# Kernel tuning notes

Hardware: AMD Instinct MI355X
Metric: run time of the kernel (lower is better)

## Reference

```python
import jax, jax.numpy as jnp
import numpy as np

DIM = 256
NUM_HEADS = 8
HEAD_DIM = DIM // NUM_HEADS
SCALE = 1.0 / DIM ** 0.5  # NOTE: source scales by 1/sqrt(dim), not 1/sqrt(head_dim)


def setup_inputs() -> dict:
    key = jax.random.key(0)
    k_x, k_wqkv, k_wout = jax.random.split(key, 3)
    x = jax.random.normal(k_x, (4, 2048, DIM), dtype=jnp.float32)
    # xavier_uniform for Linear(dim, 3*dim): limit = sqrt(6/(fan_in+fan_out))
    lim_qkv = float(np.sqrt(6.0 / (DIM + 3 * DIM)))
    w_qkv = jax.random.uniform(k_wqkv, (3 * DIM, DIM), minval=-lim_qkv, maxval=lim_qkv, dtype=jnp.float32)
    b_qkv = jnp.zeros((3 * DIM,), dtype=jnp.float32)
    lim_out = float(np.sqrt(6.0 / (DIM + DIM)))
    w_out = jax.random.uniform(k_wout, (DIM, DIM), minval=-lim_out, maxval=lim_out, dtype=jnp.float32)
    b_out = jnp.zeros((DIM,), dtype=jnp.float32)
    return {"x": x, "w_qkv": w_qkv, "b_qkv": b_qkv, "w_out": w_out, "b_out": b_out}


def reference(x, w_qkv, b_qkv, w_out, b_out):
    B, N, C = x.shape
    H, D = NUM_HEADS, C // NUM_HEADS
    qkv = x @ w_qkv.T + b_qkv                       # [B, N, 3C]
    qkv = qkv.reshape(B, N, 3, H, D)
    q = qkv[:, :, 0].transpose(0, 2, 1, 3)          # [B, H, N, D]
    k = qkv[:, :, 1].transpose(0, 2, 1, 3)
    v = qkv[:, :, 2].transpose(0, 2, 1, 3)
    attn = jnp.einsum("bhnd,bhmd->bhnm", q, k) * SCALE  # [B, H, N, N]
    attn = jax.nn.softmax(attn, axis=-1)
    z = jnp.einsum("bhnm,bhmd->bhnd", attn, v)      # [B, H, N, D]
    z = z.transpose(0, 2, 1, 3).reshape(B, N, C)
    return z @ w_out.T + b_out
```

## Files before the change

kernel.cpp:

```cpp
#include <hip/hip_runtime.h>


#define SEQ 2048
#define BATCH 4
#define NHEADS 8
#define HDIM 32
#define DIMC 256
#define SCALE_LOG2E 0.09016844005556021f

typedef __attribute__((ext_vector_type(8))) short short8;
typedef __attribute__((ext_vector_type(4))) float f32x4;

union BF8 { unsigned u[4]; short8 s8; };

__device__ __forceinline__ unsigned pk2bf(float a, float b) {
    union { float f; unsigned u; } ua, ub;
    ua.f = a; ub.f = b;
    return __builtin_amdgcn_perm(ub.u + 0x8000u, ua.u + 0x8000u, 0x07060302u);
}
__device__ __forceinline__ short f2bf(float a) {
    union { float f; unsigned u; } x; x.f = a;
    return (short)((x.u + 0x8000u) >> 16);
}

__global__ __launch_bounds__(256) void qkv_fused(const float* __restrict__ X,
                                                 const float* __restrict__ W,
                                                 const float* __restrict__ bias,
                                                 short* __restrict__ Q,
                                                 short* __restrict__ Kd,
                                                 short* __restrict__ V) {
    __shared__ __align__(16) union SM {
        struct { short A[128][72]; short B[64][72]; } ab;
        short CQ[128][72];
        short CV[64][136];
    } sm;

    const int m0 = blockIdx.y * 128, bx = blockIdx.x;
    const int n0 = bx * 64;
    const int tid = threadIdx.x;
    const int w = tid >> 6, lane = tid & 63;
    const int m = lane & 15, g = lane >> 4;
    const int wr = w >> 1, wc = w & 1;

    const int arow = tid >> 1, acol = (tid & 1) * 32;
    const int brow = tid >> 2, bcol = (tid & 3) * 16;

    f32x4 acc[4][2] = {};

    for (int kt = 0; kt < DIMC; kt += 64) {
        const float* xp = &X[(size_t)(m0 + arow) * DIMC + kt + acol];
        const float* wp = &W[(size_t)(n0 + brow) * DIMC + kt + bcol];
        float4 xv[8], wv[4];
#pragma unroll
        for (int i = 0; i < 8; i++) xv[i] = *(const float4*)(xp + i * 4);
#pragma unroll
        for (int i = 0; i < 4; i++) wv[i] = *(const float4*)(wp + i * 4);
        __syncthreads();
#pragma unroll
        for (int i = 0; i < 4; i++) {
            BF8 c;
            c.u[0] = pk2bf(xv[i * 2].x, xv[i * 2].y);
            c.u[1] = pk2bf(xv[i * 2].z, xv[i * 2].w);
            c.u[2] = pk2bf(xv[i * 2 + 1].x, xv[i * 2 + 1].y);
            c.u[3] = pk2bf(xv[i * 2 + 1].z, xv[i * 2 + 1].w);
            *(short8*)&sm.ab.A[arow][acol + i * 8] = c.s8;
        }
#pragma unroll
        for (int i = 0; i < 2; i++) {
            BF8 c;
            c.u[0] = pk2bf(wv[i * 2].x, wv[i * 2].y);
            c.u[1] = pk2bf(wv[i * 2].z, wv[i * 2].w);
            c.u[2] = pk2bf(wv[i * 2 + 1].x, wv[i * 2 + 1].y);
            c.u[3] = pk2bf(wv[i * 2 + 1].z, wv[i * 2 + 1].w);
            *(short8*)&sm.ab.B[brow][bcol + i * 8] = c.s8;
        }
        __syncthreads();
#pragma unroll
        for (int kk = 0; kk < 2; kk++) {
            short8 af[4], bf[2];
#pragma unroll
            for (int mt = 0; mt < 4; mt++)
                af[mt] = *(const short8*)&sm.ab.A[wr * 64 + mt * 16 + m][kk * 32 + g * 8];
#pragma unroll
            for (int nt = 0; nt < 2; nt++)
                bf[nt] = *(const short8*)&sm.ab.B[wc * 32 + nt * 16 + m][kk * 32 + g * 8];
#pragma unroll
            for (int mt = 0; mt < 4; mt++)
#pragma unroll
                for (int nt = 0; nt < 2; nt++)
                    acc[mt][nt] = __builtin_amdgcn_mfma_f32_16x16x32_bf16(af[mt], bf[nt], acc[mt][nt], 0, 0, 0);
        }
    }

    const int which = bx >> 2;
    const int h0 = (bx & 3) * 2;
    const int bidx = blockIdx.y >> 4;
    const int ntok0 = (blockIdx.y & 15) * 128;
    float bv[2];
#pragma unroll
    for (int nt = 0; nt < 2; nt++) bv[nt] = bias[n0 + wc * 32 + nt * 16 + m];

    __syncthreads();
    if (which != 2) {
        const float qs = (which == 0) ? SCALE_LOG2E : 1.0f;
#pragma unroll
        for (int mt = 0; mt < 4; mt++)
#pragma unroll
            for (int nt = 0; nt < 2; nt++)
#pragma unroll
                for (int r = 0; r < 4; r++)
                    sm.CQ[wr * 64 + mt * 16 + g * 4 + r][wc * 32 + nt * 16 + m] =
                        f2bf((acc[mt][nt][r] + bv[nt]) * qs);
        __syncthreads();
        short* dst = (which == 0) ? Q : Kd;
        const int tok = tid >> 1, d0 = (tid & 1) * 16;
#pragma unroll
        for (int hh = 0; hh < 2; hh++) {
            size_t o = ((size_t)((bidx * NHEADS + h0 + hh) * SEQ) + ntok0 + tok) * HDIM + d0;
            *(short8*)&dst[o] = *(const short8*)&sm.CQ[tok][hh * 32 + d0];
            *(short8*)&dst[o + 8] = *(const short8*)&sm.CQ[tok][hh * 32 + d0 + 8];
        }
    } else {
#pragma unroll
        for (int mt = 0; mt < 4; mt++)
#pragma unroll
            for (int nt = 0; nt < 2; nt++) {
                uint2 p;
                p.x = pk2bf(acc[mt][nt][0] + bv[nt], acc[mt][nt][1] + bv[nt]);
                p.y = pk2bf(acc[mt][nt][2] + bv[nt], acc[mt][nt][3] + bv[nt]);
                *(uint2*)&sm.CV[wc * 32 + nt * 16 + m][wr * 64 + mt * 16 + g * 4] = p;
            }
        __syncthreads();
        const int col = tid >> 2, t0 = (tid & 3) * 32;
        const int hh = col >> 5, d = col & 31;
        size_t o = ((size_t)((bidx * NHEADS + h0 + hh) * HDIM) + d) * SEQ + ntok0 + t0;
#pragma unroll
        for (int c2 = 0; c2 < 4; c2++)
            *(short8*)&V[o + c2 * 8] = *(const short8*)&sm.CV[col][t0 + c2 * 8];
    }
}

__global__ __launch_bounds__(256) void attn_tile(const short* __restrict__ Q,
                                                 const short* __restrict__ K,
                                                 const short* __restrict__ V,
                                                 short* __restrict__ Zb) {
    __shared__ __align__(16) union SM {
        struct { short Ks[2][128][40]; short Vs[2][32][136]; } kv;
        struct { float O[4][64][36]; float L[4][64]; } ep;
    } sm;

    const int bh = blockIdx.y;
    const int b = bh >> 3, h = bh & 7;
    const int q0 = blockIdx.x * 64;
    const short* qb = Q + (size_t)bh * SEQ * HDIM;
    const short* kb = K + (size_t)bh * SEQ * HDIM;
    const short* vb = V + (size_t)bh * HDIM * SEQ;
    const int tid = threadIdx.x;
    const int w = tid >> 6, lane = tid & 63;
    const int m = lane & 15, g = lane >> 4;

    short8 qfr[4];
#pragma unroll
    for (int qt = 0; qt < 4; qt++)
        qfr[qt] = *(const short8*)(qb + (size_t)(q0 + qt * 16 + m) * HDIM + g * 8);

    const int krow = tid >> 1, kcol = (tid & 1) * 16;
    const int rl = krow & 31;
    const int lrow = (krow & ~31) | (((rl >> 2) & 1) << 4) | ((rl >> 3) << 2) | (rl & 3);
    const int vrow = tid >> 3, vcol = (tid & 7) * 16;

    f32x4 o[4][2] = {};
    f32x4 ol[4] = {};
    const short8 ones = {0x3F80, 0x3F80, 0x3F80, 0x3F80, 0x3F80, 0x3F80, 0x3F80, 0x3F80};

    short8 k0a = *(const short8*)(kb + (size_t)krow * HDIM + kcol);
    short8 k0b = *(const short8*)(kb + (size_t)krow * HDIM + kcol + 8);
    short8 v0a = *(const short8*)(vb + (size_t)vrow * SEQ + vcol);
    short8 v0b = *(const short8*)(vb + (size_t)vrow * SEQ + vcol + 8);
    *(short8*)&sm.kv.Ks[0][lrow][kcol] = k0a;
    *(short8*)&sm.kv.Ks[0][lrow][kcol + 8] = k0b;
    *(short8*)&sm.kv.Vs[0][vrow][vcol] = v0a;
    *(short8*)&sm.kv.Vs[0][vrow][vcol + 8] = v0b;
    __syncthreads();

    for (int it = 0; it < SEQ / 128; ++it) {
        const int buf = it & 1;
        if (it < SEQ / 128 - 1) {
            const int kn = (it + 1) * 128;
            k0a = *(const short8*)(kb + (size_t)(kn + krow) * HDIM + kcol);
            k0b = *(const short8*)(kb + (size_t)(kn + krow) * HDIM + kcol + 8);
            v0a = *(const short8*)(vb + (size_t)vrow * SEQ + kn + vcol);
            v0b = *(const short8*)(vb + (size_t)vrow * SEQ + kn + vcol + 8);
        }

        short8 kf0 = *(const short8*)&sm.kv.Ks[buf][w * 32 + m][g * 8];
        short8 kf1 = *(const short8*)&sm.kv.Ks[buf][w * 32 + 16 + m][g * 8];
        short8 vf0 = *(const short8*)&sm.kv.Vs[buf][m][w * 32 + g * 8];
        short8 vf1 = *(const short8*)&sm.kv.Vs[buf][16 + m][w * 32 + g * 8];

#pragma unroll
        for (int qt = 0; qt < 4; qt++) {
            f32x4 z4 = {0.f, 0.f, 0.f, 0.f};
            f32x4 st0 = __builtin_amdgcn_mfma_f32_16x16x32_bf16(kf0, qfr[qt], z4, 0, 0, 0);
            f32x4 st1 = __builtin_amdgcn_mfma_f32_16x16x32_bf16(kf1, qfr[qt], z4, 0, 0, 0);
            BF8 a;
            a.u[0] = pk2bf(__builtin_amdgcn_exp2f(st0[0]), __builtin_amdgcn_exp2f(st0[1]));
            a.u[1] = pk2bf(__builtin_amdgcn_exp2f(st0[2]), __builtin_amdgcn_exp2f(st0[3]));
            a.u[2] = pk2bf(__builtin_amdgcn_exp2f(st1[0]), __builtin_amdgcn_exp2f(st1[1]));
            a.u[3] = pk2bf(__builtin_amdgcn_exp2f(st1[2]), __builtin_amdgcn_exp2f(st1[3]));
            o[qt][0] = __builtin_amdgcn_mfma_f32_16x16x32_bf16(a.s8, vf0, o[qt][0], 0, 0, 0);
            o[qt][1] = __builtin_amdgcn_mfma_f32_16x16x32_bf16(a.s8, vf1, o[qt][1], 0, 0, 0);
            ol[qt] = __builtin_amdgcn_mfma_f32_16x16x32_bf16(a.s8, ones, ol[qt], 0, 0, 0);
        }

        if (it < SEQ / 128 - 1) {
            const int nb = buf ^ 1;
            *(short8*)&sm.kv.Ks[nb][lrow][kcol] = k0a;
            *(short8*)&sm.kv.Ks[nb][lrow][kcol + 8] = k0b;
            *(short8*)&sm.kv.Vs[nb][vrow][vcol] = v0a;
            *(short8*)&sm.kv.Vs[nb][vrow][vcol + 8] = v0b;
        }
        __syncthreads();
    }

#pragma unroll
    for (int qt = 0; qt < 4; qt++) {
#pragma unroll
        for (int dh = 0; dh < 2; dh++)
#pragma unroll
            for (int r = 0; r < 4; r++)
                sm.ep.O[w][qt * 16 + g * 4 + r][dh * 16 + m] = o[qt][dh][r];
        if (m == 0)
#pragma unroll
            for (int r = 0; r < 4; r++)
                sm.ep.L[w][qt * 16 + g * 4 + r] = ol[qt][r];
    }
    __syncthreads();

    const int ql = tid >> 2, d0 = (tid & 3) * 8;
    float lt = sm.ep.L[0][ql] + sm.ep.L[1][ql] + sm.ep.L[2][ql] + sm.ep.L[3][ql];
    float inv = __builtin_amdgcn_rcpf(lt);
    float sv[8];
#pragma unroll
    for (int j = 0; j < 8; j++)
        sv[j] = sm.ep.O[0][ql][d0 + j] + sm.ep.O[1][ql][d0 + j] +
                sm.ep.O[2][ql][d0 + j] + sm.ep.O[3][ql][d0 + j];
    BF8 pz;
#pragma unroll
    for (int j = 0; j < 4; j++)
        pz.u[j] = pk2bf(sv[2 * j] * inv, sv[2 * j + 1] * inv);
    *(short8*)&Zb[(size_t)(b * SEQ + q0 + ql) * DIMC + h * HDIM + d0] = pz.s8;
}

__global__ __launch_bounds__(256) void out_fused(const short* __restrict__ A,
                                                 const float* __restrict__ W,
                                                 const float* __restrict__ bias,
                                                 float* __restrict__ C) {
    __shared__ __align__(16) short As[64][72];
    __shared__ __align__(16) short Bs[64][72];
    const int m0 = blockIdx.y * 64, n0 = blockIdx.x * 64;
    const int tid = threadIdx.x;
    const int w = tid >> 6, lane = tid & 63;
    const int m = lane & 15, g = lane >> 4;
    const int srow = tid >> 2, scol = (tid & 3) * 16;

    f32x4 acc[4] = {};

    for (int kt = 0; kt < DIMC; kt += 64) {
        short8 a0 = *(const short8*)&A[(size_t)(m0 + srow) * DIMC + kt + scol];
        short8 a1 = *(const short8*)&A[(size_t)(m0 + srow) * DIMC + kt + scol + 8];
        const float* wp = &W[(size_t)(n0 + srow) * DIMC + kt + scol];
        float4 wv[4];
#pragma unroll
        for (int i = 0; i < 4; i++) wv[i] = *(const float4*)(wp + i * 4);
        __syncthreads();
        *(short8*)&As[srow][scol] = a0;
        *(short8*)&As[srow][scol + 8] = a1;
#pragma unroll
        for (int i = 0; i < 2; i++) {
            BF8 c;
            c.u[0] = pk2bf(wv[i * 2].x, wv[i * 2].y);
            c.u[1] = pk2bf(wv[i * 2].z, wv[i * 2].w);
            c.u[2] = pk2bf(wv[i * 2 + 1].x, wv[i * 2 + 1].y);
            c.u[3] = pk2bf(wv[i * 2 + 1].z, wv[i * 2 + 1].w);
            *(short8*)&Bs[srow][scol + i * 8] = c.s8;
        }
        __syncthreads();
#pragma unroll
        for (int kk = 0; kk < 2; kk++) {
            short8 af = *(const short8*)&As[w * 16 + m][kk * 32 + g * 8];
#pragma unroll
            for (int nt = 0; nt < 4; nt++) {
                short8 bf = *(const short8*)&Bs[nt * 16 + m][kk * 32 + g * 8];
                acc[nt] = __builtin_amdgcn_mfma_f32_16x16x32_bf16(af, bf, acc[nt], 0, 0, 0);
            }
        }
    }

    float bv[4];
#pragma unroll
    for (int nt = 0; nt < 4; nt++) bv[nt] = bias[n0 + nt * 16 + m];
#pragma unroll
    for (int nt = 0; nt < 4; nt++)
#pragma unroll
        for (int r = 0; r < 4; r++)
            C[(size_t)(m0 + w * 16 + g * 4 + r) * DIMC + n0 + nt * 16 + m] = acc[nt][r] + bv[nt];
}

extern "C" void kernel_launch(void* const* d_in, const int* in_sizes, int n_in,
                              void* d_out, int out_size, void* d_ws, size_t ws_size,
                              hipStream_t stream) {
    const float* x     = (const float*)d_in[0];
    const float* w_qkv = (const float*)d_in[1];
    const float* b_qkv = (const float*)d_in[2];
    const float* w_out = (const float*)d_in[3];
    const float* b_out = (const float*)d_in[4];
    float* out = (float*)d_out;

    const size_t HSZ = (size_t)BATCH * NHEADS * SEQ * HDIM;
    short* qw = (short*)d_ws;
    short* kw = qw + HSZ;
    short* vw = kw + HSZ;
    short* zb = vw + HSZ;

    qkv_fused<<<dim3(12, 64), 256, 0, stream>>>(x, w_qkv, b_qkv, qw, kw, vw);
    attn_tile<<<dim3(32, 32), 256, 0, stream>>>(qw, kw, vw, zb);
    out_fused<<<dim3(4, 128), 256, 0, stream>>>(zb, w_out, b_out, out);
}
```

Baseline: 131.7 us.

## Pre-convert inputs and weights to bf16 and register-prefetch GEMM tiles

Adds a separate kernel that converts x, w_qkv and w_out to bf16 once, so the QKV and output GEMMs load bf16 directly instead of converting fp32 inside every tile. Both GEMMs now prefetch the next K tile into registers while the current tile is computed, overlapping global loads with MFMA work. This costs an extra launch plus an fp32 read and bf16 write of x (about 8 MB of traffic), which could outweigh the per-tile conversion it removes, since x is read by 12 column blocks in the QKV kernel.

Measured after the change: 120.0 us. -8.9%, faster.

```diff
diff --git a/kernel.cpp b/kernel.cpp
--- a/kernel.cpp
+++ b/kernel.cpp
@@ -23,12 +23,36 @@
     return (short)((x.u + 0x8000u) >> 16);
 }
 
-__global__ __launch_bounds__(256) void qkv_fused(const float* __restrict__ X,
-                                                 const float* __restrict__ W,
-                                                 const float* __restrict__ bias,
-                                                 short* __restrict__ Q,
-                                                 short* __restrict__ Kd,
-                                                 short* __restrict__ V) {
+#define NX (BATCH * SEQ * DIMC)
+#define NQW (3 * DIMC * DIMC)
+#define NOW (DIMC * DIMC)
+
+__global__ __launch_bounds__(256) void cvt_bf16(const float* __restrict__ x,
+                                                const float* __restrict__ wq,
+                                                const float* __restrict__ wo,
+                                                short* __restrict__ xb,
+                                                short* __restrict__ wqb,
+                                                short* __restrict__ wob) {
+    int i = (blockIdx.x * 256 + threadIdx.x) * 4;
+    const float* src;
+    short* dst;
+    int off;
+    if (i < NX) { src = x; dst = xb; off = i; }
+    else if (i < NX + NQW) { src = wq; dst = wqb; off = i - NX; }
+    else { src = wo; dst = wob; off = i - NX - NQW; }
+    float4 v = *(const float4*)&src[off];
+    uint2 p;
+    p.x = pk2bf(v.x, v.y);
+    p.y = pk2bf(v.z, v.w);
+    *(uint2*)&dst[off] = p;
+}
+
+__global__ __launch_bounds__(256) void qkv_mfma(const short* __restrict__ Xb,
+                                                const short* __restrict__ Wb,
+                                                const float* __restrict__ bias,
+                                                short* __restrict__ Q,
+                                                short* __restrict__ Kd,
+                                                short* __restrict__ V) {
     __shared__ __align__(16) union SM {
         struct { short A[128][72]; short B[64][72]; } ab;
         short CQ[128][72];
@@ -47,34 +71,28 @@
 
     f32x4 acc[4][2] = {};
 
+    const short* ap = Xb + (size_t)(m0 + arow) * DIMC + acol;
+    const short* bp = Wb + (size_t)(n0 + brow) * DIMC + bcol;
+
+    short8 pa[4], pb[2];
+#pragma unroll
+    for (int i = 0; i < 4; i++) pa[i] = *(const short8*)(ap + i * 8);
+#pragma unroll
+    for (int i = 0; i < 2; i++) pb[i] = *(const short8*)(bp + i * 8);
+
     for (int kt = 0; kt < DIMC; kt += 64) {
-        const float* xp = &X[(size_t)(m0 + arow) * DIMC + kt + acol];
-        const float* wp = &W[(size_t)(n0 + brow) * DIMC + kt + bcol];
-        float4 xv[8], wv[4];
-#pragma unroll
-        for (int i = 0; i < 8; i++) xv[i] = *(const float4*)(xp + i * 4);
-#pragma unroll
-        for (int i = 0; i < 4; i++) wv[i] = *(const float4*)(wp + i * 4);
-        __syncthreads();
-#pragma unroll
-        for (int i = 0; i < 4; i++) {
-            BF8 c;
-            c.u[0] = pk2bf(xv[i * 2].x, xv[i * 2].y);
-            c.u[1] = pk2bf(xv[i * 2].z, xv[i * 2].w);
-            c.u[2] = pk2bf(xv[i * 2 + 1].x, xv[i * 2 + 1].y);
-            c.u[3] = pk2bf(xv[i * 2 + 1].z, xv[i * 2 + 1].w);
-            *(short8*)&sm.ab.A[arow][acol + i * 8] = c.s8;
-        }
-#pragma unroll
-        for (int i = 0; i < 2; i++) {
-            BF8 c;
-            c.u[0] = pk2bf(wv[i * 2].x, wv[i * 2].y);
-            c.u[1] = pk2bf(wv[i * 2].z, wv[i * 2].w);
-            c.u[2] = pk2bf(wv[i * 2 + 1].x, wv[i * 2 + 1].y);
-            c.u[3] = pk2bf(wv[i * 2 + 1].z, wv[i * 2 + 1].w);
-            *(short8*)&sm.ab.B[brow][bcol + i * 8] = c.s8;
-        }
-        __syncthreads();
+        __syncthreads();
+#pragma unroll
+        for (int i = 0; i < 4; i++) *(short8*)&sm.ab.A[arow][acol + i * 8] = pa[i];
+#pragma unroll
+        for (int i = 0; i < 2; i++) *(short8*)&sm.ab.B[brow][bcol + i * 8] = pb[i];
+        __syncthreads();
+        if (kt + 64 < DIMC) {
+#pragma unroll
+            for (int i = 0; i < 4; i++) pa[i] = *(const short8*)(ap + kt + 64 + i * 8);
+#pragma unroll
+            for (int i = 0; i < 2; i++) pb[i] = *(const short8*)(bp + kt + 64 + i * 8);
+        }
 #pragma unroll
         for (int kk = 0; kk < 2; kk++) {
             short8 af[4], bf[2];
@@ -252,10 +270,10 @@
     *(short8*)&Zb[(size_t)(b * SEQ + q0 + ql) * DIMC + h * HDIM + d0] = pz.s8;
 }
 
-__global__ __launch_bounds__(256) void out_fused(const short* __restrict__ A,
-                                                 const float* __restrict__ W,
-                                                 const float* __restrict__ bias,
-                                                 float* __restrict__ C) {
+__global__ __launch_bounds__(256) void out_mfma(const short* __restrict__ A,
+                                                const short* __restrict__ Wb,
+                                                const float* __restrict__ bias,
+                                                float* __restrict__ C) {
     __shared__ __align__(16) short As[64][72];
     __shared__ __align__(16) short Bs[64][72];
     const int m0 = blockIdx.y * 64, n0 = blockIdx.x * 64;
@@ -266,26 +284,31 @@
 
     f32x4 acc[4] = {};
 
+    const short* ap = A + (size_t)(m0 + srow) * DIMC + scol;
+    const short* bp = Wb + (size_t)(n0 + srow) * DIMC + scol;
+
+    short8 pa[2], pb[2];
+#pragma unroll
+    for (int i = 0; i < 2; i++) {
+        pa[i] = *(const short8*)(ap + i * 8);
+        pb[i] = *(const short8*)(bp + i * 8);
+    }
+
     for (int kt = 0; kt < DIMC; kt += 64) {
-        short8 a0 = *(const short8*)&A[(size_t)(m0 + srow) * DIMC + kt + scol];
-        short8 a1 = *(const short8*)&A[(size_t)(m0 + srow) * DIMC + kt + scol + 8];
-        const float* wp = &W[(size_t)(n0 + srow) * DIMC + kt + scol];
-        float4 wv[4];
-#pragma unroll
-        for (int i = 0; i < 4; i++) wv[i] = *(const float4*)(wp + i * 4);
-        __syncthreads();
-        *(short8*)&As[srow][scol] = a0;
-        *(short8*)&As[srow][scol + 8] = a1;
+        __syncthreads();
 #pragma unroll
         for (int i = 0; i < 2; i++) {
-            BF8 c;
-            c.u[0] = pk2bf(wv[i * 2].x, wv[i * 2].y);
-            c.u[1] = pk2bf(wv[i * 2].z, wv[i * 2].w);
-            c.u[2] = pk2bf(wv[i * 2 + 1].x, wv[i * 2 + 1].y);
-            c.u[3] = pk2bf(wv[i * 2 + 1].z, wv[i * 2 + 1].w);
-            *(short8*)&Bs[srow][scol + i * 8] = c.s8;
-        }
-        __syncthreads();
+            *(short8*)&As[srow][scol + i * 8] = pa[i];
+            *(short8*)&Bs[srow][scol + i * 8] = pb[i];
+        }
+        __syncthreads();
+        if (kt + 64 < DIMC) {
+#pragma unroll
+            for (int i = 0; i < 2; i++) {
+                pa[i] = *(const short8*)(ap + kt + 64 + i * 8);
+                pb[i] = *(const short8*)(bp + kt + 64 + i * 8);
+            }
+        }
 #pragma unroll
         for (int kk = 0; kk < 2; kk++) {
             short8 af = *(const short8*)&As[w * 16 + m][kk * 32 + g * 8];
@@ -318,12 +341,16 @@
     float* out = (float*)d_out;
 
     const size_t HSZ = (size_t)BATCH * NHEADS * SEQ * HDIM;
-    short* qw = (short*)d_ws;
-    short* kw = qw + HSZ;
-    short* vw = kw + HSZ;
-    short* zb = vw + HSZ;
-
-    qkv_fused<<<dim3(12, 64), 256, 0, stream>>>(x, w_qkv, b_qkv, qw, kw, vw);
+    short* xb  = (short*)d_ws;
+    short* wqb = xb + NX;
+    short* wob = wqb + NQW;
+    short* qw  = wob + NOW;
+    short* kw  = qw + HSZ;
+    short* vw  = kw + HSZ;
+    short* zb  = vw + HSZ;
+
+    cvt_bf16<<<(NX + NQW + NOW) / 1024, 256, 0, stream>>>(x, w_qkv, w_out, xb, wqb, wob);
+    qkv_mfma<<<dim3(12, 64), 256, 0, stream>>>(xb, wqb, b_qkv, qw, kw, vw);
     attn_tile<<<dim3(32, 32), 256, 0, stream>>>(qw, kw, vw, zb);
-    out_fused<<<dim3(4, 128), 256, 0, stream>>>(zb, w_out, b_out, out);
-}
+    out_mfma<<<dim3(4, 128), 256, 0, stream>>>(zb, wob, b_out, out);
+}
```
